# Performance work log

Measured on AMD Instinct MI355X. Metric: run time of the kernel, lower is better.

## Reference

```python
import jax, jax.numpy as jnp
import numpy as np

B, S, W = 32, 256, 32
T = 16               # topics per doc, each spanning L = S//T sentences
VOCAB, E, H, D = 400001, 300, 128, 128


def _gru_scan(x, Wih, Whh, bih, bhh, reverse=False):
    """x: [B,S,E] -> (outputs [B,S,H], final hidden [B,H]). Torch GRU cell math."""
    h0 = jnp.zeros((x.shape[0], Whh.shape[1]), x.dtype)
    gi_all = jnp.einsum('bse,ge->bsg', x, Wih) + bih  # precompute input gates [B,S,3H]

    def step(h, gi):
        gh = h @ Whh.T + bhh
        ir, iz, inn = jnp.split(gi, 3, axis=-1)
        hr, hz, hn = jnp.split(gh, 3, axis=-1)
        r = jax.nn.sigmoid(ir + hr)
        z = jax.nn.sigmoid(iz + hz)
        n = jnp.tanh(inn + r * hn)
        h_new = (1.0 - z) * n + z * h
        return h_new, h_new

    hT, hs = jax.lax.scan(step, h0, jnp.swapaxes(gi_all, 0, 1), reverse=reverse)
    return jnp.swapaxes(hs, 0, 1), hT


def setup_inputs() -> dict:
    key = jax.random.key(0)
    ks = jax.random.split(key, 16)
    sc_i = 1.0 / np.sqrt(H)
    L = S // T
    starts = (jnp.arange(T, dtype=jnp.int32) * L + 1)          # 1-based inclusive
    ends = (jnp.arange(T, dtype=jnp.int32) + 1) * L
    tse = jnp.broadcast_to(jnp.stack([starts, ends], axis=-1)[None], (B, T, 2)).astype(jnp.int32)
    return {
        'word_ids': jax.random.randint(ks[0], (B, S, W), 0, VOCAB, dtype=jnp.int32),
        'topic_start_ends': tse,
        'embed_table': jax.random.normal(ks[1], (VOCAB, E), jnp.float32) * 0.6,
        'Wih_f': jax.random.normal(ks[2], (3 * H, E), jnp.float32) * sc_i,
        'Whh_f': jax.random.normal(ks[3], (3 * H, H), jnp.float32) * sc_i,
        'bih_f': jax.random.normal(ks[4], (3 * H,), jnp.float32) * sc_i,
        'bhh_f': jax.random.normal(ks[5], (3 * H,), jnp.float32) * sc_i,
        'Wih_b': jax.random.normal(ks[6], (3 * H, E), jnp.float32) * sc_i,
        'Whh_b': jax.random.normal(ks[7], (3 * H, H), jnp.float32) * sc_i,
        'bih_b': jax.random.normal(ks[8], (3 * H,), jnp.float32) * sc_i,
        'bhh_b': jax.random.normal(ks[9], (3 * H,), jnp.float32) * sc_i,
        'v_attention': jax.random.normal(ks[10], (4 * H, 1), jnp.float32),
        'W_attention': jax.random.normal(ks[11], (4 * H, 4 * H), jnp.float32) * (1.0 / np.sqrt(4 * H)),
        'W1': jax.random.normal(ks[12], (D, 4 * H), jnp.float32) * (1.0 / np.sqrt(4 * H)),
        'b1': jax.random.normal(ks[13], (D,), jnp.float32) * 0.01,
        'W2': jax.random.normal(ks[14], (1, D), jnp.float32) * (1.0 / np.sqrt(D)),
        'b2': jax.random.normal(ks[15], (1,), jnp.float32) * 0.01,
    }


def reference(word_ids, topic_start_ends, embed_table,
              Wih_f, Whh_f, bih_f, bhh_f, Wih_b, Whh_b, bih_b, bhh_b,
              v_attention, W_attention, W1, b1, W2, b2):
    b, s, _ = word_ids.shape
    h = Whh_f.shape[1]
    # --- sent_encoder: gather word embeddings, mean-pool per sentence ---
    sent_emb = jnp.mean(embed_table[word_ids], axis=2)          # [B,S,E]
    # --- doc_encoder: bi-GRU ---
    out_f, hT_f = _gru_scan(sent_emb, Wih_f, Whh_f, bih_f, bhh_f, reverse=False)
    out_b, hT_b = _gru_scan(sent_emb, Wih_b, Whh_b, bih_b, bhh_b, reverse=True)
    sent_rep = jnp.concatenate([out_f, out_b], axis=-1)         # [B,S,2H]
    # faithful to hidden.view(batch_size, 2H) on hidden of shape [2,B,H]
    doc_vec = jnp.stack([hT_f, hT_b], axis=0).reshape(b, 2 * h)
    doc_rep = jnp.broadcast_to(doc_vec[:, None, :], (b, s, 2 * h))
    # topic reps via segment difference of cumulative GRU states (pad trick)
    pad = jnp.pad(sent_rep, ((0, 0), (1, 1), (0, 0)))           # [B,S+2,2H]
    starts = topic_start_ends[:, :, 0]                          # [B,T], 1-based
    ends = topic_start_ends[:, :, 1]

    def gat(idx, lo, hi):
        return jnp.take_along_axis(pad[..., lo:hi], idx[:, :, None], axis=1)
    fwd_part = gat(ends, 0, h) - gat(starts - 1, 0, h)
    bwd_part = gat(starts, h, 2 * h) - gat(ends + 1, h, 2 * h)
    topic_mat = jnp.concatenate([fwd_part, bwd_part], axis=-1)  # [B,T,2H]
    # scatter topic vectors to sentences: topic id = #starts at or before sentence
    sidx = jnp.arange(s, dtype=starts.dtype)
    topic_id = jnp.sum(sidx[None, :, None] >= (starts - 1)[:, None, :], axis=-1) - 1  # [B,S]
    topic_rep = jnp.take_along_axis(topic_mat, topic_id[:, :, None], axis=1)          # [B,S,2H]
    # --- decoder ---
    cat_ds = jnp.concatenate([doc_rep, sent_rep], axis=-1)      # [B,S,4H]
    cat_ts = jnp.concatenate([topic_rep, sent_rep], axis=-1)
    doc_scores = jnp.tanh(cat_ds @ W_attention) @ v_attention   # [B,S,1]
    topic_scores = jnp.tanh(cat_ts @ W_attention) @ v_attention
    doc_w = jax.nn.softmax(doc_scores, axis=1)
    topic_w = jax.nn.softmax(topic_scores, axis=1)
    context = doc_w * doc_rep + topic_w * topic_rep             # [B,S,2H]
    inp = jnp.concatenate([sent_rep, context], axis=-1)         # [B,S,4H]
    hdd = jax.nn.relu(inp @ W1.T + b1)                          # dropout = identity (eval)
    logits = (hdd @ W2.T + b2).squeeze(-1)                      # [B,S]
    return logits
```

## Files before the change

kernel.cpp:

```cpp
#include <hip/hip_runtime.h>
#include <hip/hip_bf16.h>
#include <cstdint>

#define Bk 32
#define Sk 256
#define Wk 32
#define Tk 16
#define Ek 300
#define Hk 128
#define Dk 128
#define NROWS (Bk*Sk)
#define GI_N  (3*Hk*2)
#define KPAD  320

typedef __attribute__((ext_vector_type(8))) short short8v;
typedef __attribute__((ext_vector_type(4))) float f32x4;

__device__ __forceinline__ float fast_sigmoid(float x) {
    return 1.f / (1.f + __expf(-x));
}
__device__ __forceinline__ float fast_tanh(float x) {
    float ax = fabsf(x);
    float e = __expf(2.f * ax);
    float t = 1.f - 2.f / (1.f + e);
    return copysignf(t, x);
}
__device__ __forceinline__ void barrier_lgkm() {
    asm volatile("s_waitcnt lgkmcnt(0)" ::: "memory");
    __builtin_amdgcn_s_barrier();
}
__device__ __forceinline__ void fma44(const float4& a, const float4& b, float (&c)[4][4]) {
    c[0][0]=fmaf(a.x,b.x,c[0][0]); c[0][1]=fmaf(a.x,b.y,c[0][1]); c[0][2]=fmaf(a.x,b.z,c[0][2]); c[0][3]=fmaf(a.x,b.w,c[0][3]);
    c[1][0]=fmaf(a.y,b.x,c[1][0]); c[1][1]=fmaf(a.y,b.y,c[1][1]); c[1][2]=fmaf(a.y,b.z,c[1][2]); c[1][3]=fmaf(a.y,b.w,c[1][3]);
    c[2][0]=fmaf(a.z,b.x,c[2][0]); c[2][1]=fmaf(a.z,b.y,c[2][1]); c[2][2]=fmaf(a.z,b.z,c[2][2]); c[2][3]=fmaf(a.z,b.w,c[2][3]);
    c[3][0]=fmaf(a.w,b.x,c[3][0]); c[3][1]=fmaf(a.w,b.y,c[3][1]); c[3][2]=fmaf(a.w,b.z,c[3][2]); c[3][3]=fmaf(a.w,b.w,c[3][3]);
}
__device__ __forceinline__ unsigned short f2bf(float f) {
    uint32_t u = __float_as_uint(f);
    uint32_t r = (u + 0x7FFFu + ((u >> 16) & 1u)) >> 16;
    return (unsigned short)r;
}
__device__ __forceinline__ float bf2f(unsigned short h) {
    return __uint_as_float(((uint32_t)h) << 16);
}

__global__ __launch_bounds__(256) void pack_kernel(
    const float* __restrict__ Wf, const float* __restrict__ Wb,
    const float* __restrict__ bf, const float* __restrict__ bb,
    const float* __restrict__ Watt, const float* __restrict__ W1,
    unsigned short* __restrict__ Bgt_hi, unsigned short* __restrict__ Bgt_lo,
    float* __restrict__ bias_gi, unsigned short* __restrict__ Wswt,
    float* __restrict__ BW1)
{
    int idx = blockIdx.x * 256 + threadIdx.x;
    if (idx < 768 * KPAD) {
        int n = idx / KPAD, k = idx % KPAD;
        float v = 0.f;
        if (k < 300) v = (n < 384) ? Wf[n * 300 + k] : Wb[(n - 384) * 300 + k];
        unsigned short h = f2bf(v);
        Bgt_hi[idx] = h;
        Bgt_lo[idx] = f2bf(v - bf2f(h));
    }
    if (idx < 768) bias_gi[idx] = (idx < 384) ? bf[idx] : bb[idx - 384];
    if (idx < 512 * 256) {
        int n = idx >> 8, k = idx & 255;
        Wswt[idx] = f2bf(Watt[(size_t)(256 + k) * 512 + n]);
    }
    if (idx < 512 * 128) {
        int k = idx >> 7, n = idx & 127;
        BW1[idx] = W1[n * 512 + k];
    }
}

__global__ __launch_bounds__(256) void embed_mean_kernel(
    const int* __restrict__ wids, const float* __restrict__ table,
    unsigned short* __restrict__ Ahi, unsigned short* __restrict__ Alo)
{
    int wv = (blockIdx.x << 2) + (threadIdx.x >> 6);
    int lane = threadIdx.x & 63;
    if (wv >= NROWS) return;
    const int* idp = wids + (size_t)wv * Wk;
    float4 a0 = {0,0,0,0}, a1 = {0,0,0,0};
    #pragma unroll 4
    for (int w = 0; w < Wk; ++w) {
        int id = idp[w];
        const float4* r4 = reinterpret_cast<const float4*>(table + (size_t)id * Ek);
        float4 v0 = r4[lane];
        a0.x += v0.x; a0.y += v0.y; a0.z += v0.z; a0.w += v0.w;
        if (lane < 11) {
            float4 v1 = r4[64 + lane];
            a1.x += v1.x; a1.y += v1.y; a1.z += v1.z; a1.w += v1.w;
        }
    }
    const float sc = 1.f / 32.f;
    unsigned short* hp = Ahi + (size_t)wv * KPAD;
    unsigned short* lp = Alo + (size_t)wv * KPAD;
    {
        float v[4] = {a0.x*sc, a0.y*sc, a0.z*sc, a0.w*sc};
        ushort4 h, l;
        h.x=f2bf(v[0]); h.y=f2bf(v[1]); h.z=f2bf(v[2]); h.w=f2bf(v[3]);
        l.x=f2bf(v[0]-bf2f(h.x)); l.y=f2bf(v[1]-bf2f(h.y));
        l.z=f2bf(v[2]-bf2f(h.z)); l.w=f2bf(v[3]-bf2f(h.w));
        *reinterpret_cast<ushort4*>(hp + lane*4) = h;
        *reinterpret_cast<ushort4*>(lp + lane*4) = l;
    }
    if (lane < 11) {
        float v[4] = {a1.x*sc, a1.y*sc, a1.z*sc, a1.w*sc};
        ushort4 h, l;
        h.x=f2bf(v[0]); h.y=f2bf(v[1]); h.z=f2bf(v[2]); h.w=f2bf(v[3]);
        l.x=f2bf(v[0]-bf2f(h.x)); l.y=f2bf(v[1]-bf2f(h.y));
        l.z=f2bf(v[2]-bf2f(h.z)); l.w=f2bf(v[3]-bf2f(h.w));
        *reinterpret_cast<ushort4*>(hp + 256 + lane*4) = h;
        *reinterpret_cast<ushort4*>(lp + 256 + lane*4) = l;
    } else if (lane < 16) {
        ushort4 z = {0,0,0,0};
        *reinterpret_cast<ushort4*>(hp + 256 + lane*4) = z;
        *reinterpret_cast<ushort4*>(lp + 256 + lane*4) = z;
    }
}

__global__ __launch_bounds__(256) void cvt_bf16_kernel(
    const float* __restrict__ src, unsigned short* __restrict__ dst, int n8)
{
    int i = blockIdx.x * 256 + threadIdx.x;
    if (i >= n8) return;
    const float4* s = reinterpret_cast<const float4*>(src) + (size_t)i * 2;
    float4 v0 = s[0], v1 = s[1];
    unsigned short r[8];
    r[0]=f2bf(v0.x); r[1]=f2bf(v0.y); r[2]=f2bf(v0.z); r[3]=f2bf(v0.w);
    r[4]=f2bf(v1.x); r[5]=f2bf(v1.y); r[6]=f2bf(v1.z); r[7]=f2bf(v1.w);
    *reinterpret_cast<short8v*>(dst + (size_t)i * 8) = *reinterpret_cast<short8v*>(r);
}

template<int PASSES, bool BIAS>
__global__ __launch_bounds__(256) void mfma_gemm_kernel(
    const unsigned short* __restrict__ Ahi, const unsigned short* __restrict__ Alo,
    const unsigned short* __restrict__ Bthi, const unsigned short* __restrict__ Btlo,
    const float* __restrict__ bias, float* __restrict__ C,
    int M, int N, int Kp)
{
    __shared__ unsigned short At_h[128][40];
    __shared__ unsigned short Bt_h[128][40];
    __shared__ unsigned short At_l[128][40];
    __shared__ unsigned short Bt_l[128][40];
    const int tid = threadIdx.x;
    const int m0 = blockIdx.x * 128, n0 = blockIdx.y * 128;
    const int lane = tid & 63;
    const int wave = tid >> 6;
    const int wr = (wave >> 1) * 64, wc = (wave & 1) * 64;
    const int l15 = lane & 15, l4 = lane >> 4;
    f32x4 acc[4][4] = {};

    const int srow = tid >> 1;
    const int scol = (tid & 1) * 16;

    for (int k0 = 0; k0 < Kp; k0 += 32) {
        {
            const unsigned short* ag = Ahi + (size_t)(m0 + srow) * Kp + k0 + scol;
            *reinterpret_cast<short8v*>(&At_h[srow][scol])     = *reinterpret_cast<const short8v*>(ag);
            *reinterpret_cast<short8v*>(&At_h[srow][scol + 8]) = *reinterpret_cast<const short8v*>(ag + 8);
            const unsigned short* bg = Bthi + (size_t)(n0 + srow) * Kp + k0 + scol;
            *reinterpret_cast<short8v*>(&Bt_h[srow][scol])     = *reinterpret_cast<const short8v*>(bg);
            *reinterpret_cast<short8v*>(&Bt_h[srow][scol + 8]) = *reinterpret_cast<const short8v*>(bg + 8);
            if (PASSES > 1) {
                const unsigned short* ag2 = Alo + (size_t)(m0 + srow) * Kp + k0 + scol;
                *reinterpret_cast<short8v*>(&At_l[srow][scol])     = *reinterpret_cast<const short8v*>(ag2);
                *reinterpret_cast<short8v*>(&At_l[srow][scol + 8]) = *reinterpret_cast<const short8v*>(ag2 + 8);
                const unsigned short* bg2 = Btlo + (size_t)(n0 + srow) * Kp + k0 + scol;
                *reinterpret_cast<short8v*>(&Bt_l[srow][scol])     = *reinterpret_cast<const short8v*>(bg2);
                *reinterpret_cast<short8v*>(&Bt_l[srow][scol + 8]) = *reinterpret_cast<const short8v*>(bg2 + 8);
            }
        }
        __syncthreads();
        short8v a_h[4], b_h[4], a_l[4], b_l[4];
        #pragma unroll
        for (int f = 0; f < 4; ++f) {
            a_h[f] = *reinterpret_cast<const short8v*>(&At_h[wr + f*16 + l15][l4*8]);
            b_h[f] = *reinterpret_cast<const short8v*>(&Bt_h[wc + f*16 + l15][l4*8]);
            if (PASSES > 1) {
                a_l[f] = *reinterpret_cast<const short8v*>(&At_l[wr + f*16 + l15][l4*8]);
                b_l[f] = *reinterpret_cast<const short8v*>(&Bt_l[wc + f*16 + l15][l4*8]);
            }
        }
        #pragma unroll
        for (int i = 0; i < 4; ++i) {
            #pragma unroll
            for (int j = 0; j < 4; ++j) {
                acc[i][j] = __builtin_amdgcn_mfma_f32_16x16x32_bf16(a_h[i], b_h[j], acc[i][j], 0, 0, 0);
                if (PASSES > 1) {
                    acc[i][j] = __builtin_amdgcn_mfma_f32_16x16x32_bf16(a_l[i], b_h[j], acc[i][j], 0, 0, 0);
                    acc[i][j] = __builtin_amdgcn_mfma_f32_16x16x32_bf16(a_h[i], b_l[j], acc[i][j], 0, 0, 0);
                }
            }
        }
        __syncthreads();
    }
    #pragma unroll
    for (int i = 0; i < 4; ++i) {
        #pragma unroll
        for (int j = 0; j < 4; ++j) {
            int col = n0 + wc + j * 16 + l15;
            float badd = BIAS ? bias[col] : 0.f;
            #pragma unroll
            for (int r = 0; r < 4; ++r) {
                int row = m0 + wr + i * 16 + l4 * 4 + r;
                C[(size_t)row * N + col] = acc[i][j][r] + badd;
            }
        }
    }
}

template<bool BIAS, bool RELU>
__global__ __launch_bounds__(256) void gemm_kernel(
    const float* __restrict__ A, const float* __restrict__ B,
    const float* __restrict__ bias, float* __restrict__ C,
    int M, int N, int K)
{
    __shared__ float As[64][68];
    __shared__ float Bs[64][68];
    const int tid = threadIdx.x;
    const int m0 = blockIdx.x * 64;
    const int n0 = blockIdx.y * 64;
    const int tx = tid & 15, ty = tid >> 4;
    const int lr = tid >> 2;
    const int lc = tid & 3;
    float acc[4][4] = {};

    for (int k0 = 0; k0 < K; k0 += 64) {
        #pragma unroll
        for (int i = 0; i < 4; ++i) {
            int kk = lc * 4 + i * 16;
            int gm = m0 + lr;
            int gk = k0 + kk;
            float4 v = {0,0,0,0};
            if (gm < M && gk < K)
                v = *reinterpret_cast<const float4*>(A + (size_t)gm * K + gk);
            As[kk+0][lr] = v.x; As[kk+1][lr] = v.y; As[kk+2][lr] = v.z; As[kk+3][lr] = v.w;
        }
        #pragma unroll
        for (int i = 0; i < 4; ++i) {
            int nn = lc * 4 + i * 16;
            int gk = k0 + lr;
            float4 v = {0,0,0,0};
            if (gk < K)
                v = *reinterpret_cast<const float4*>(B + (size_t)gk * N + n0 + nn);
            *reinterpret_cast<float4*>(&Bs[lr][nn]) = v;
        }
        __syncthreads();
        #pragma unroll 8
        for (int k = 0; k < 64; ++k) {
            float4 av = *reinterpret_cast<const float4*>(&As[k][ty*4]);
            float4 bv = *reinterpret_cast<const float4*>(&Bs[k][tx*4]);
            fma44(av, bv, acc);
        }
        __syncthreads();
    }
    #pragma unroll
    for (int r = 0; r < 4; ++r) {
        int row = m0 + ty * 4 + r;
        if (row < M) {
            float4 v = {acc[r][0], acc[r][1], acc[r][2], acc[r][3]};
            if (BIAS) {
                const float* bp = bias + n0 + tx * 4;
                v.x += bp[0]; v.y += bp[1]; v.z += bp[2]; v.w += bp[3];
            }
            if (RELU) {
                v.x = fmaxf(v.x, 0.f); v.y = fmaxf(v.y, 0.f);
                v.z = fmaxf(v.z, 0.f); v.w = fmaxf(v.w, 0.f);
            }
            *reinterpret_cast<float4*>(C + (size_t)row * N + n0 + tx * 4) = v;
        }
    }
}

__global__ __launch_bounds__(512, 1) void gru_scan_kernel(
    const float* __restrict__ gi,
    const float* __restrict__ Whh_f, const float* __restrict__ Whh_b,
    const float* __restrict__ bhh_f, const float* __restrict__ bhh_b,
    float* __restrict__ sent_rep,
    float* __restrict__ hT)
{
    const int blk = blockIdx.x;
    const int dir = blk >> 5;
    const int b   = blk & 31;
    const int t = threadIdx.x;
    const int lane = t & 63;
    const int w_id = t >> 6;
    const int q = lane >> 4;
    const int m = lane & 15;
    const int j = w_id * 16 + m;
    const float* Whh = dir ? Whh_b : Whh_f;
    const float* bhh = dir ? bhh_b : bhh_f;
    __shared__ float hbufA[144];
    __shared__ float hbufB[144];

    const float* wr0 = Whh + (size_t)j * 128 + 32 * q;
    const float* wr1 = wr0 + 128 * 128;
    const float* wr2 = wr0 + 256 * 128;
    float4 wA0 = *reinterpret_cast<const float4*>(wr0 +  0);
    float4 wA1 = *reinterpret_cast<const float4*>(wr0 +  4);
    float4 wA2 = *reinterpret_cast<const float4*>(wr0 +  8);
    float4 wA3 = *reinterpret_cast<const float4*>(wr0 + 12);
    float4 wA4 = *reinterpret_cast<const float4*>(wr0 + 16);
    float4 wA5 = *reinterpret_cast<const float4*>(wr0 + 20);
    float4 wA6 = *reinterpret_cast<const float4*>(wr0 + 24);
    float4 wA7 = *reinterpret_cast<const float4*>(wr0 + 28);
    float4 wB0 = *reinterpret_cast<const float4*>(wr1 +  0);
    float4 wB1 = *reinterpret_cast<const float4*>(wr1 +  4);
    float4 wB2 = *reinterpret_cast<const float4*>(wr1 +  8);
    float4 wB3 = *reinterpret_cast<const float4*>(wr1 + 12);
    float4 wB4 = *reinterpret_cast<const float4*>(wr1 + 16);
    float4 wB5 = *reinterpret_cast<const float4*>(wr1 + 20);
    float4 wB6 = *reinterpret_cast<const float4*>(wr1 + 24);
    float4 wB7 = *reinterpret_cast<const float4*>(wr1 + 28);
    float4 wC0 = *reinterpret_cast<const float4*>(wr2 +  0);
    float4 wC1 = *reinterpret_cast<const float4*>(wr2 +  4);
    float4 wC2 = *reinterpret_cast<const float4*>(wr2 +  8);
    float4 wC3 = *reinterpret_cast<const float4*>(wr2 + 12);
    float4 wC4 = *reinterpret_cast<const float4*>(wr2 + 16);
    float4 wC5 = *reinterpret_cast<const float4*>(wr2 + 20);
    float4 wC6 = *reinterpret_cast<const float4*>(wr2 + 24);
    float4 wC7 = *reinterpret_cast<const float4*>(wr2 + 28);
    const float br = bhh[j];
    const float bz = bhh[128 + j];
    const float bn = bhh[256 + j];

    if (t < 144) { hbufA[t] = 0.f; hbufB[t] = 0.f; }

    const int ji = 36 * (j >> 5) + (j & 31);
    const float* gbase = gi + (size_t)(b * Sk) * GI_N + dir * 384 + j;
    float hold = 0.f;
    float gir = 0.f, giz = 0.f, gin_ = 0.f;
    {
        const int s0 = dir ? (Sk - 1) : 0;
        const float* gp = gbase + (size_t)s0 * GI_N;
        gir = gp[0]; giz = gp[128]; gin_ = gp[256];
    }
    __syncthreads();

    #define STEP(RD, WR, SEXPR) { \
        const int s = (SEXPR); \
        const float4* hseg = reinterpret_cast<const float4*>(RD) + 9 * q; \
        float pA = 0.f, pB = 0.f, pC = 0.f; \
        { float4 h4; \
          h4 = hseg[0]; \
          pA=fmaf(wA0.x,h4.x,pA); pA=fmaf(wA0.y,h4.y,pA); pA=fmaf(wA0.z,h4.z,pA); pA=fmaf(wA0.w,h4.w,pA); \
          pB=fmaf(wB0.x,h4.x,pB); pB=fmaf(wB0.y,h4.y,pB); pB=fmaf(wB0.z,h4.z,pB); pB=fmaf(wB0.w,h4.w,pB); \
          pC=fmaf(wC0.x,h4.x,pC); pC=fmaf(wC0.y,h4.y,pC); pC=fmaf(wC0.z,h4.z,pC); pC=fmaf(wC0.w,h4.w,pC); \
          h4 = hseg[1]; \
          pA=fmaf(wA1.x,h4.x,pA); pA=fmaf(wA1.y,h4.y,pA); pA=fmaf(wA1.z,h4.z,pA); pA=fmaf(wA1.w,h4.w,pA); \
          pB=fmaf(wB1.x,h4.x,pB); pB=fmaf(wB1.y,h4.y,pB); pB=fmaf(wB1.z,h4.z,pB); pB=fmaf(wB1.w,h4.w,pB); \
          pC=fmaf(wC1.x,h4.x,pC); pC=fmaf(wC1.y,h4.y,pC); pC=fmaf(wC1.z,h4.z,pC); pC=fmaf(wC1.w,h4.w,pC); \
          h4 = hseg[2]; \
          pA=fmaf(wA2.x,h4.x,pA); pA=fmaf(wA2.y,h4.y,pA); pA=fmaf(wA2.z,h4.z,pA); pA=fmaf(wA2.w,h4.w,pA); \
          pB=fmaf(wB2.x,h4.x,pB); pB=fmaf(wB2.y,h4.y,pB); pB=fmaf(wB2.z,h4.z,pB); pB=fmaf(wB2.w,h4.w,pB); \
          pC=fmaf(wC2.x,h4.x,pC); pC=fmaf(wC2.y,h4.y,pC); pC=fmaf(wC2.z,h4.z,pC); pC=fmaf(wC2.w,h4.w,pC); \
          h4 = hseg[3]; \
          pA=fmaf(wA3.x,h4.x,pA); pA=fmaf(wA3.y,h4.y,pA); pA=fmaf(wA3.z,h4.z,pA); pA=fmaf(wA3.w,h4.w,pA); \
          pB=fmaf(wB3.x,h4.x,pB); pB=fmaf(wB3.y,h4.y,pB); pB=fmaf(wB3.z,h4.z,pB); pB=fmaf(wB3.w,h4.w,pB); \
          pC=fmaf(wC3.x,h4.x,pC); pC=fmaf(wC3.y,h4.y,pC); pC=fmaf(wC3.z,h4.z,pC); pC=fmaf(wC3.w,h4.w,pC); \
          h4 = hseg[4]; \
          pA=fmaf(wA4.x,h4.x,pA); pA=fmaf(wA4.y,h4.y,pA); pA=fmaf(wA4.z,h4.z,pA); pA=fmaf(wA4.w,h4.w,pA); \
          pB=fmaf(wB4.x,h4.x,pB); pB=fmaf(wB4.y,h4.y,pB); pB=fmaf(wB4.z,h4.z,pB); pB=fmaf(wB4.w,h4.w,pB); \
          pC=fmaf(wC4.x,h4.x,pC); pC=fmaf(wC4.y,h4.y,pC); pC=fmaf(wC4.z,h4.z,pC); pC=fmaf(wC4.w,h4.w,pC); \
          h4 = hseg[5]; \
          pA=fmaf(wA5.x,h4.x,pA); pA=fmaf(wA5.y,h4.y,pA); pA=fmaf(wA5.z,h4.z,pA); pA=fmaf(wA5.w,h4.w,pA); \
          pB=fmaf(wB5.x,h4.x,pB); pB=fmaf(wB5.y,h4.y,pB); pB=fmaf(wB5.z,h4.z,pB); pB=fmaf(wB5.w,h4.w,pB); \
          pC=fmaf(wC5.x,h4.x,pC); pC=fmaf(wC5.y,h4.y,pC); pC=fmaf(wC5.z,h4.z,pC); pC=fmaf(wC5.w,h4.w,pC); \
          h4 = hseg[6]; \
          pA=fmaf(wA6.x,h4.x,pA); pA=fmaf(wA6.y,h4.y,pA); pA=fmaf(wA6.z,h4.z,pA); pA=fmaf(wA6.w,h4.w,pA); \
          pB=fmaf(wB6.x,h4.x,pB); pB=fmaf(wB6.y,h4.y,pB); pB=fmaf(wB6.z,h4.z,pB); pB=fmaf(wB6.w,h4.w,pB); \
          pC=fmaf(wC6.x,h4.x,pC); pC=fmaf(wC6.y,h4.y,pC); pC=fmaf(wC6.z,h4.z,pC); pC=fmaf(wC6.w,h4.w,pC); \
          h4 = hseg[7]; \
          pA=fmaf(wA7.x,h4.x,pA); pA=fmaf(wA7.y,h4.y,pA); pA=fmaf(wA7.z,h4.z,pA); pA=fmaf(wA7.w,h4.w,pA); \
          pB=fmaf(wB7.x,h4.x,pB); pB=fmaf(wB7.y,h4.y,pB); pB=fmaf(wB7.z,h4.z,pB); pB=fmaf(wB7.w,h4.w,pB); \
          pC=fmaf(wC7.x,h4.x,pC); pC=fmaf(wC7.y,h4.y,pC); pC=fmaf(wC7.z,h4.z,pC); pC=fmaf(wC7.w,h4.w,pC); } \
        pA += __shfl_xor(pA, 16); pA += __shfl_xor(pA, 32); \
        pB += __shfl_xor(pB, 16); pB += __shfl_xor(pB, 32); \
        pC += __shfl_xor(pC, 16); pC += __shfl_xor(pC, 32); \
        if (q == 0) { \
            float r = fast_sigmoid(gir + pA + br); \
            float z = fast_sigmoid(giz + pB + bz); \
            float n = fast_tanh(gin_ + r * (pC + bn)); \
            hold = (1.f - z) * n + z * hold; \
            (WR)[ji] = hold; \
            sent_rep[(size_t)(b * Sk + s) * 256 + dir * 128 + j] = hold; \
            const int sn = dir ? (s > 0 ? s - 1 : 0) : (s + 1 < Sk ? s + 1 : Sk - 1); \
            const float* gp = gbase + (size_t)sn * GI_N; \
            gir = gp[0]; giz = gp[128]; gin_ = gp[256]; \
        } \
        barrier_lgkm(); \
    }

    for (int step = 0; step < Sk; step += 2) {
        STEP(hbufA, hbufB, dir ? (Sk - 1 - step) : step);
        STEP(hbufB, hbufA, dir ? (Sk - 2 - step) : (step + 1));
    }
    #undef STEP

    if (q == 0) hT[dir * 4096 + b * 128 + j] = hold;
}

__device__ __forceinline__ float4 sr_load_guard(const float* sr, int b, int sidx, int j4) {
    if (sidx < 0 || sidx >= Sk) { float4 z = {0,0,0,0}; return z; }
    return reinterpret_cast<const float4*>(sr)[(size_t)(b * Sk + sidx) * 64 + j4];
}
__global__ __launch_bounds__(64) void prep_kernel(
    const int* __restrict__ tse, const float* __restrict__ sent_rep,
    const float* __restrict__ hT, float* __restrict__ dvtm)
{
    const int b = blockIdx.x;
    const int t = blockIdx.y;
    const int j4 = threadIdx.x;
    if (t == 16) {
        int dir = b >> 4;
        int bb = 2 * (b & 15) + (j4 >> 5);
        int jj4 = j4 & 31;
        float4 v = reinterpret_cast<const float4*>(hT)[dir * 1024 + bb * 32 + jj4];
        reinterpret_cast<float4*>(dvtm)[b * 64 + j4] = v;
    } else {
        int st = tse[b * 32 + t * 2];
        int en = tse[b * 32 + t * 2 + 1];
        float4 va, vb;
        if (j4 < 32) {
            va = sr_load_guard(sent_rep, b, en - 1, j4);
            vb = sr_load_guard(sent_rep, b, st - 2, j4);
        } else {
            va = sr_load_guard(sent_rep, b, st - 1, j4);
            vb = sr_load_guard(sent_rep, b, en, j4);
        }
        float4 v = {va.x - vb.x, va.y - vb.y, va.z - vb.z, va.w - vb.w};
        reinterpret_cast<float4*>(dvtm)[(32 + b * 16 + t) * 64 + j4] = v;
    }
}

__global__ __launch_bounds__(256) void scores_kernel(
    const float* __restrict__ SW,
    const float* __restrict__ dptp,
    const float* __restrict__ vatt,
    const int* __restrict__ tse,
    float* __restrict__ dsc, float* __restrict__ tsc)
{
    int row = (blockIdx.x << 2) + (threadIdx.x >> 6);
    int lane = threadIdx.x & 63;
    if (row >= NROWS) return;
    int b = row >> 8, s = row & 255;
    int ti = 0;
    #pragma unroll
    for (int t = 1; t < 16; ++t) ti += (s >= tse[b * 32 + t * 2] - 1) ? 1 : 0;
    const float4* swr = reinterpret_cast<const float4*>(SW + (size_t)row * 512);
    const float4* dpr = reinterpret_cast<const float4*>(dptp + (size_t)b * 512);
    const float4* tpr = reinterpret_cast<const float4*>(dptp + (size_t)(32 + b * 16 + ti) * 512);
    const float4* vv  = reinterpret_cast<const float4*>(vatt);
    float sd = 0.f, st = 0.f;
    #pragma unroll
    for (int q = 0; q < 2; ++q) {
        int i = lane * 2 + q;
        float4 sw = swr[i], dp = dpr[i], tp = tpr[i], v = vv[i];
        sd += fast_tanh(sw.x + dp.x) * v.x + fast_tanh(sw.y + dp.y) * v.y
            + fast_tanh(sw.z + dp.z) * v.z + fast_tanh(sw.w + dp.w) * v.w;
        st += fast_tanh(sw.x + tp.x) * v.x + fast_tanh(sw.y + tp.y) * v.y
            + fast_tanh(sw.z + tp.z) * v.z + fast_tanh(sw.w + tp.w) * v.w;
    }
    #pragma unroll
    for (int off = 32; off; off >>= 1) {
        sd += __shfl_xor(sd, off);
        st += __shfl_xor(st, off);
    }
    if (lane == 0) { dsc[row] = sd; tsc[row] = st; }
}

__global__ __launch_bounds__(256) void softmax_kernel(float* __restrict__ dsc, float* __restrict__ tsc)
{
    const int b = blockIdx.x, sidx = threadIdx.x;
    const int lane = sidx & 63, wid = sidx >> 6;
    __shared__ float rd[4], rt[4];
    float d = dsc[b * Sk + sidx];
    float t = tsc[b * Sk + sidx];
    float md = d, mt = t;
    #pragma unroll
    for (int off = 32; off; off >>= 1) {
        md = fmaxf(md, __shfl_xor(md, off));
        mt = fmaxf(mt, __shfl_xor(mt, off));
    }
    if (lane == 0) { rd[wid] = md; rt[wid] = mt; }
    __syncthreads();
    md = fmaxf(fmaxf(rd[0], rd[1]), fmaxf(rd[2], rd[3]));
    mt = fmaxf(fmaxf(rt[0], rt[1]), fmaxf(rt[2], rt[3]));
    float ed = __expf(d - md), et = __expf(t - mt);
    float sd = ed, stt = et;
    #pragma unroll
    for (int off = 32; off; off >>= 1) {
        sd += __shfl_xor(sd, off);
        stt += __shfl_xor(stt, off);
    }
    __syncthreads();
    if (lane == 0) { rd[wid] = sd; rt[wid] = stt; }
    __syncthreads();
    sd = rd[0] + rd[1] + rd[2] + rd[3];
    stt = rt[0] + rt[1] + rt[2] + rt[3];
    dsc[b * Sk + sidx] = ed / sd;
    tsc[b * Sk + sidx] = et / stt;
}

__global__ __launch_bounds__(128) void build_inp_kernel(
    const float* __restrict__ sent_rep, const float* __restrict__ dvtm,
    const float* __restrict__ dw, const float* __restrict__ tw,
    const int* __restrict__ tse, float* __restrict__ inp)
{
    int row = blockIdx.x;
    int b = row >> 8, s = row & 255;
    int f4c = threadIdx.x;
    float4 v;
    if (f4c < 64) {
        v = reinterpret_cast<const float4*>(sent_rep)[(size_t)row * 64 + f4c];
    } else {
        int ti = 0;
        #pragma unroll
        for (int t = 1; t < 16; ++t) ti += (s >= tse[b * 32 + t * 2] - 1) ? 1 : 0;
        float dwv = dw[row], twv = tw[row];
        int j4 = f4c - 64;
        float4 dv = reinterpret_cast<const float4*>(dvtm)[b * 64 + j4];
        float4 tm = reinterpret_cast<const float4*>(dvtm)[(32 + b * 16 + ti) * 64 + j4];
        v.x = dwv * dv.x + twv * tm.x;
        v.y = dwv * dv.y + twv * tm.y;
        v.z = dwv * dv.z + twv * tm.z;
        v.w = dwv * dv.w + twv * tm.w;
    }
    reinterpret_cast<float4*>(inp)[(size_t)row * 128 + f4c] = v;
}

__global__ __launch_bounds__(256) void logits_kernel(
    const float* __restrict__ hdd, const float* __restrict__ W2,
    const float* __restrict__ b2, float* __restrict__ out)
{
    int row = (blockIdx.x << 2) + (threadIdx.x >> 6);
    int lane = threadIdx.x & 63;
    if (row >= NROWS) return;
    float acc = hdd[(size_t)row * 128 + lane] * W2[lane]
              + hdd[(size_t)row * 128 + 64 + lane] * W2[64 + lane];
    #pragma unroll
    for (int off = 32; off; off >>= 1) acc += __shfl_xor(acc, off);
    if (lane == 0) out[row] = acc + b2[0];
}

extern "C" void kernel_launch(void* const* d_in, const int* in_sizes, int n_in,
                              void* d_out, int out_size, void* d_ws, size_t ws_size,
                              hipStream_t stream)
{
    const int*   wids  = (const int*)d_in[0];
    const int*   tse   = (const int*)d_in[1];
    const float* table = (const float*)d_in[2];
    const float* Wihf  = (const float*)d_in[3];
    const float* Whhf  = (const float*)d_in[4];
    const float* bihf  = (const float*)d_in[5];
    const float* bhhf  = (const float*)d_in[6];
    const float* Wihb  = (const float*)d_in[7];
    const float* Whhb  = (const float*)d_in[8];
    const float* bihb  = (const float*)d_in[9];
    const float* bhhb  = (const float*)d_in[10];
    const float* vatt  = (const float*)d_in[11];
    const float* Watt  = (const float*)d_in[12];
    const float* W1    = (const float*)d_in[13];
    const float* b1    = (const float*)d_in[14];
    const float* W2    = (const float*)d_in[15];
    const float* b2    = (const float*)d_in[16];
    float* ws = (float*)d_ws;
    float* out = (float*)d_out;

    unsigned short* Ahi   = (unsigned short*)(ws + 0);
    unsigned short* Alo   = (unsigned short*)(ws + 1310720);
    float* gi             = ws + 2621440;
    float* sent_rep       = ws + 8912896;
    unsigned short* SRhi  = (unsigned short*)(ws + 11010048);
    float* hT             = ws + 12058624;
    float* dvtm           = ws + 12066816;
    float* dptp           = ws + 12206080;
    float* dsc            = ws + 12484608;
    float* tsc            = ws + 12492800;
    unsigned short* BgtH  = (unsigned short*)(ws + 12500992);
    unsigned short* BgtL  = (unsigned short*)(ws + 12623872);
    float* bias_gi        = ws + 12746752;
    unsigned short* Wswt  = (unsigned short*)(ws + 12747520);
    float* BW1            = ws + 12813056;
    float* SW             = ws + 12878592;
    float* inp            = ws + 0;
    float* hdd            = ws + 4194304;

    if (ws_size < (size_t)17072896 * sizeof(float)) return;

    pack_kernel<<<960, 256, 0, stream>>>(Wihf, Wihb, bihf, bihb, Watt, W1,
                                         BgtH, BgtL, bias_gi, Wswt, BW1);
    embed_mean_kernel<<<2048, 256, 0, stream>>>(wids, table, Ahi, Alo);
    mfma_gemm_kernel<3, true><<<dim3(64, 6), 256, 0, stream>>>(
        Ahi, Alo, BgtH, BgtL, bias_gi, gi, NROWS, 768, KPAD);
    gru_scan_kernel<<<64, 512, 0, stream>>>(gi, Whhf, Whhb, bhhf, bhhb, sent_rep, hT);
    cvt_bf16_kernel<<<1024, 256, 0, stream>>>(sent_rep, SRhi, NROWS * 256 / 8);
    prep_kernel<<<dim3(32, 17), 64, 0, stream>>>(tse, sent_rep, hT, dvtm);
    mfma_gemm_kernel<1, false><<<dim3(64, 4), 256, 0, stream>>>(
        SRhi, nullptr, Wswt, nullptr, nullptr, SW, NROWS, 512, 256);
    gemm_kernel<false,false><<<dim3(9, 8), 256, 0, stream>>>(dvtm, Watt, nullptr, dptp, 544, 512, 256);
    scores_kernel<<<2048, 256, 0, stream>>>(SW, dptp, vatt, tse, dsc, tsc);
    softmax_kernel<<<32, 256, 0, stream>>>(dsc, tsc);
    build_inp_kernel<<<NROWS, 128, 0, stream>>>(sent_rep, dvtm, dsc, tsc, tse, inp);
    gemm_kernel<true,true><<<dim3(128, 2), 256, 0, stream>>>(inp, BW1, b1, hdd, NROWS, 128, 512);
    logits_kernel<<<2048, 256, 0, stream>>>(hdd, W2, b2, out);
}
```

Before: 345.6 us.

## Fuse attention score epilogue into MFMA GEMM and move W1 GEMM to split-bf16 MFMA

The SW=sent_rep·W_att GEMM now computes tanh-and-dot with v_attention directly in its epilogue. It writes per-slot partial doc and topic scores, so the 8192x512 fp32 SW matrix is never written and read back. The softmax sums the 8 partials. The final W1 layer switches from the fp32 SIMT GEMM to a 3-pass hi/lo bf16 MFMA GEMM with fused bias and ReLU, and build_inp emits split bf16 inputs. A small kernel precomputes the topic-id map once instead of recomputing it in several kernels. The W1 GEMM launches only 64 blocks, which may underfill the GPU.

```diff
diff --git a/kernel.cpp b/kernel.cpp
--- a/kernel.cpp
+++ b/kernel.cpp
@@ -50,7 +50,7 @@
     const float* __restrict__ Watt, const float* __restrict__ W1,
     unsigned short* __restrict__ Bgt_hi, unsigned short* __restrict__ Bgt_lo,
     float* __restrict__ bias_gi, unsigned short* __restrict__ Wswt,
-    float* __restrict__ BW1)
+    unsigned short* __restrict__ W1H, unsigned short* __restrict__ W1L)
 {
     int idx = blockIdx.x * 256 + threadIdx.x;
     if (idx < 768 * KPAD) {
@@ -66,9 +66,11 @@
         int n = idx >> 8, k = idx & 255;
         Wswt[idx] = f2bf(Watt[(size_t)(256 + k) * 512 + n]);
     }
-    if (idx < 512 * 128) {
-        int k = idx >> 7, n = idx & 127;
-        BW1[idx] = W1[n * 512 + k];
+    if (idx < 128 * 512) {
+        float v = W1[idx];
+        unsigned short h = f2bf(v);
+        W1H[idx] = h;
+        W1L[idx] = f2bf(v - bf2f(h));
     }
 }
 
@@ -132,7 +134,7 @@
     *reinterpret_cast<short8v*>(dst + (size_t)i * 8) = *reinterpret_cast<short8v*>(r);
 }
 
-template<int PASSES, bool BIAS>
+template<int PASSES, bool BIAS, bool RELU>
 __global__ __launch_bounds__(256) void mfma_gemm_kernel(
     const unsigned short* __restrict__ Ahi, const unsigned short* __restrict__ Alo,
     const unsigned short* __restrict__ Bthi, const unsigned short* __restrict__ Btlo,
@@ -204,7 +206,90 @@
             #pragma unroll
             for (int r = 0; r < 4; ++r) {
                 int row = m0 + wr + i * 16 + l4 * 4 + r;
-                C[(size_t)row * N + col] = acc[i][j][r] + badd;
+                float v = acc[i][j][r] + badd;
+                if (RELU) v = fmaxf(v, 0.f);
+                C[(size_t)row * N + col] = v;
+            }
+        }
+    }
+}
+
+__global__ __launch_bounds__(256) void mfma_swscore_kernel(
+    const unsigned short* __restrict__ Ahi, const unsigned short* __restrict__ Bthi,
+    const float* __restrict__ dptp, const float* __restrict__ vatt,
+    const int* __restrict__ tidmap,
+    float* __restrict__ dscp, float* __restrict__ tscp)
+{
+    __shared__ unsigned short At_h[128][40];
+    __shared__ unsigned short Bt_h[128][40];
+    const int tid = threadIdx.x;
+    const int m0 = blockIdx.x * 128, n0 = blockIdx.y * 128;
+    const int Kp = 256, N = 512;
+    (void)N;
+    const int lane = tid & 63;
+    const int wave = tid >> 6;
+    const int wr = (wave >> 1) * 64, wc = (wave & 1) * 64;
+    const int l15 = lane & 15, l4 = lane >> 4;
+    f32x4 acc[4][4] = {};
+
+    const int srow = tid >> 1;
+    const int scol = (tid & 1) * 16;
+
+    for (int k0 = 0; k0 < Kp; k0 += 32) {
+        {
+            const unsigned short* ag = Ahi + (size_t)(m0 + srow) * Kp + k0 + scol;
+            *reinterpret_cast<short8v*>(&At_h[srow][scol])     = *reinterpret_cast<const short8v*>(ag);
+            *reinterpret_cast<short8v*>(&At_h[srow][scol + 8]) = *reinterpret_cast<const short8v*>(ag + 8);
+            const unsigned short* bg = Bthi + (size_t)(n0 + srow) * Kp + k0 + scol;
+            *reinterpret_cast<short8v*>(&Bt_h[srow][scol])     = *reinterpret_cast<const short8v*>(bg);
+            *reinterpret_cast<short8v*>(&Bt_h[srow][scol + 8]) = *reinterpret_cast<const short8v*>(bg + 8);
+        }
+        __syncthreads();
+        short8v a_h[4], b_h[4];
+        #pragma unroll
+        for (int f = 0; f < 4; ++f) {
+            a_h[f] = *reinterpret_cast<const short8v*>(&At_h[wr + f*16 + l15][l4*8]);
+            b_h[f] = *reinterpret_cast<const short8v*>(&Bt_h[wc + f*16 + l15][l4*8]);
+        }
+        #pragma unroll
+        for (int i = 0; i < 4; ++i)
+            #pragma unroll
+            for (int j = 0; j < 4; ++j)
+                acc[i][j] = __builtin_amdgcn_mfma_f32_16x16x32_bf16(a_h[i], b_h[j], acc[i][j], 0, 0, 0);
+        __syncthreads();
+    }
+    const int bb = m0 >> 8;
+    const float* dpr = dptp + (size_t)bb * 512;
+    float vv[4], dpv[4];
+    #pragma unroll
+    for (int j = 0; j < 4; ++j) {
+        int col = n0 + wc + j * 16 + l15;
+        vv[j] = vatt[col];
+        dpv[j] = dpr[col];
+    }
+    const int slot = blockIdx.y * 2 + (wc >> 6);
+    #pragma unroll
+    for (int i = 0; i < 4; ++i) {
+        #pragma unroll
+        for (int r = 0; r < 4; ++r) {
+            int row = m0 + wr + i * 16 + l4 * 4 + r;
+            int ti = tidmap[row];
+            const float* tpr = dptp + (size_t)(32 + bb * 16 + ti) * 512;
+            float sd = 0.f, st = 0.f;
+            #pragma unroll
+            for (int j = 0; j < 4; ++j) {
+                int col = n0 + wc + j * 16 + l15;
+                float c = acc[i][j][r];
+                sd += fast_tanh(c + dpv[j]) * vv[j];
+                st += fast_tanh(c + tpr[col]) * vv[j];
+            }
+            sd += __shfl_xor(sd, 1); sd += __shfl_xor(sd, 2);
+            sd += __shfl_xor(sd, 4); sd += __shfl_xor(sd, 8);
+            st += __shfl_xor(st, 1); st += __shfl_xor(st, 2);
+            st += __shfl_xor(st, 4); st += __shfl_xor(st, 8);
+            if (l15 == 0) {
+                dscp[(size_t)row * 8 + slot] = sd;
+                tscp[(size_t)row * 8 + slot] = st;
             }
         }
     }
@@ -277,8 +362,7 @@
     const float* __restrict__ gi,
     const float* __restrict__ Whh_f, const float* __restrict__ Whh_b,
     const float* __restrict__ bhh_f, const float* __restrict__ bhh_b,
-    float* __restrict__ sent_rep,
-    float* __restrict__ hT)
+    float* __restrict__ sent_rep, float* __restrict__ hT)
 {
     const int blk = blockIdx.x;
     const int dir = blk >> 5;
@@ -434,49 +518,28 @@
     }
 }
 
-__global__ __launch_bounds__(256) void scores_kernel(
-    const float* __restrict__ SW,
-    const float* __restrict__ dptp,
-    const float* __restrict__ vatt,
-    const int* __restrict__ tse,
+__global__ __launch_bounds__(256) void topic_map_kernel(
+    const int* __restrict__ tse, int* __restrict__ tidmap)
+{
+    const int b = blockIdx.x, s = threadIdx.x;
+    int ti = 0;
+    #pragma unroll
+    for (int t = 1; t < 16; ++t) ti += (s >= tse[b * 32 + t * 2] - 1) ? 1 : 0;
+    tidmap[b * 256 + s] = ti;
+}
+
+__global__ __launch_bounds__(256) void softmax_kernel(
+    const float* __restrict__ dscp, const float* __restrict__ tscp,
     float* __restrict__ dsc, float* __restrict__ tsc)
-{
-    int row = (blockIdx.x << 2) + (threadIdx.x >> 6);
-    int lane = threadIdx.x & 63;
-    if (row >= NROWS) return;
-    int b = row >> 8, s = row & 255;
-    int ti = 0;
-    #pragma unroll
-    for (int t = 1; t < 16; ++t) ti += (s >= tse[b * 32 + t * 2] - 1) ? 1 : 0;
-    const float4* swr = reinterpret_cast<const float4*>(SW + (size_t)row * 512);
-    const float4* dpr = reinterpret_cast<const float4*>(dptp + (size_t)b * 512);
-    const float4* tpr = reinterpret_cast<const float4*>(dptp + (size_t)(32 + b * 16 + ti) * 512);
-    const float4* vv  = reinterpret_cast<const float4*>(vatt);
-    float sd = 0.f, st = 0.f;
-    #pragma unroll
-    for (int q = 0; q < 2; ++q) {
-        int i = lane * 2 + q;
-        float4 sw = swr[i], dp = dpr[i], tp = tpr[i], v = vv[i];
-        sd += fast_tanh(sw.x + dp.x) * v.x + fast_tanh(sw.y + dp.y) * v.y
-            + fast_tanh(sw.z + dp.z) * v.z + fast_tanh(sw.w + dp.w) * v.w;
-        st += fast_tanh(sw.x + tp.x) * v.x + fast_tanh(sw.y + tp.y) * v.y
-            + fast_tanh(sw.z + tp.z) * v.z + fast_tanh(sw.w + tp.w) * v.w;
-    }
-    #pragma unroll
-    for (int off = 32; off; off >>= 1) {
-        sd += __shfl_xor(sd, off);
-        st += __shfl_xor(st, off);
-    }
-    if (lane == 0) { dsc[row] = sd; tsc[row] = st; }
-}
-
-__global__ __launch_bounds__(256) void softmax_kernel(float* __restrict__ dsc, float* __restrict__ tsc)
 {
     const int b = blockIdx.x, sidx = threadIdx.x;
     const int lane = sidx & 63, wid = sidx >> 6;
     __shared__ float rd[4], rt[4];
-    float d = dsc[b * Sk + sidx];
-    float t = tsc[b * Sk + sidx];
+    const float4* dp8 = reinterpret_cast<const float4*>(dscp + (size_t)(b * Sk + sidx) * 8);
+    const float4* tp8 = reinterpret_cast<const float4*>(tscp + (size_t)(b * Sk + sidx) * 8);
+    float4 d0 = dp8[0], d1 = dp8[1], t0 = tp8[0], t1 = tp8[1];
+    float d = ((d0.x + d0.y) + (d0.z + d0.w)) + ((d1.x + d1.y) + (d1.z + d1.w));
+    float t = ((t0.x + t0.y) + (t0.z + t0.w)) + ((t1.x + t1.y) + (t1.z + t1.w));
     float md = d, mt = t;
     #pragma unroll
     for (int off = 32; off; off >>= 1) {
@@ -506,18 +569,17 @@
 __global__ __launch_bounds__(128) void build_inp_kernel(
     const float* __restrict__ sent_rep, const float* __restrict__ dvtm,
     const float* __restrict__ dw, const float* __restrict__ tw,
-    const int* __restrict__ tse, float* __restrict__ inp)
+    const int* __restrict__ tidmap,
+    unsigned short* __restrict__ inpH, unsigned short* __restrict__ inpL)
 {
     int row = blockIdx.x;
-    int b = row >> 8, s = row & 255;
+    int b = row >> 8;
     int f4c = threadIdx.x;
     float4 v;
     if (f4c < 64) {
         v = reinterpret_cast<const float4*>(sent_rep)[(size_t)row * 64 + f4c];
     } else {
-        int ti = 0;
-        #pragma unroll
-        for (int t = 1; t < 16; ++t) ti += (s >= tse[b * 32 + t * 2] - 1) ? 1 : 0;
+        int ti = tidmap[row];
         float dwv = dw[row], twv = tw[row];
         int j4 = f4c - 64;
         float4 dv = reinterpret_cast<const float4*>(dvtm)[b * 64 + j4];
@@ -527,7 +589,12 @@
         v.z = dwv * dv.z + twv * tm.z;
         v.w = dwv * dv.w + twv * tm.w;
     }
-    reinterpret_cast<float4*>(inp)[(size_t)row * 128 + f4c] = v;
+    ushort4 h, l;
+    h.x = f2bf(v.x); h.y = f2bf(v.y); h.z = f2bf(v.z); h.w = f2bf(v.w);
+    l.x = f2bf(v.x - bf2f(h.x)); l.y = f2bf(v.y - bf2f(h.y));
+    l.z = f2bf(v.z - bf2f(h.z)); l.w = f2bf(v.w - bf2f(h.w));
+    *reinterpret_cast<ushort4*>(inpH + (size_t)row * 512 + f4c * 4) = h;
+    *reinterpret_cast<ushort4*>(inpL + (size_t)row * 512 + f4c * 4) = l;
 }
 
 __global__ __launch_bounds__(256) void logits_kernel(
@@ -582,27 +649,32 @@
     unsigned short* BgtL  = (unsigned short*)(ws + 12623872);
     float* bias_gi        = ws + 12746752;
     unsigned short* Wswt  = (unsigned short*)(ws + 12747520);
-    float* BW1            = ws + 12813056;
-    float* SW             = ws + 12878592;
-    float* inp            = ws + 0;
+    unsigned short* W1H   = (unsigned short*)(ws + 12813056);
+    unsigned short* W1L   = (unsigned short*)(ws + 12845824);
+    float* dscp           = ws + 12878592;
+    float* tscp           = ws + 12944128;
+    int*   tidmap         = (int*)(ws + 13009664);
+    unsigned short* inpH  = (unsigned short*)(ws + 0);
+    unsigned short* inpL  = (unsigned short*)(ws + 2097152);
     float* hdd            = ws + 4194304;
 
-    if (ws_size < (size_t)17072896 * sizeof(float)) return;
+    if (ws_size < (size_t)13017856 * sizeof(float)) return;
 
     pack_kernel<<<960, 256, 0, stream>>>(Wihf, Wihb, bihf, bihb, Watt, W1,
-                                         BgtH, BgtL, bias_gi, Wswt, BW1);
+                                         BgtH, BgtL, bias_gi, Wswt, W1H, W1L);
     embed_mean_kernel<<<2048, 256, 0, stream>>>(wids, table, Ahi, Alo);
-    mfma_gemm_kernel<3, true><<<dim3(64, 6), 256, 0, stream>>>(
+    mfma_gemm_kernel<3, true, false><<<dim3(64, 6), 256, 0, stream>>>(
         Ahi, Alo, BgtH, BgtL, bias_gi, gi, NROWS, 768, KPAD);
     gru_scan_kernel<<<64, 512, 0, stream>>>(gi, Whhf, Whhb, bhhf, bhhb, sent_rep, hT);
     cvt_bf16_kernel<<<1024, 256, 0, stream>>>(sent_rep, SRhi, NROWS * 256 / 8);
     prep_kernel<<<dim3(32, 17), 64, 0, stream>>>(tse, sent_rep, hT, dvtm);
-    mfma_gemm_kernel<1, false><<<dim3(64, 4), 256, 0, stream>>>(
-        SRhi, nullptr, Wswt, nullptr, nullptr, SW, NROWS, 512, 256);
+    topic_map_kernel<<<32, 256, 0, stream>>>(tse, tidmap);
     gemm_kernel<false,false><<<dim3(9, 8), 256, 0, stream>>>(dvtm, Watt, nullptr, dptp, 544, 512, 256);
-    scores_kernel<<<2048, 256, 0, stream>>>(SW, dptp, vatt, tse, dsc, tsc);
-    softmax_kernel<<<32, 256, 0, stream>>>(dsc, tsc);
-    build_inp_kernel<<<NROWS, 128, 0, stream>>>(sent_rep, dvtm, dsc, tsc, tse, inp);
-    gemm_kernel<true,true><<<dim3(128, 2), 256, 0, stream>>>(inp, BW1, b1, hdd, NROWS, 128, 512);
+    mfma_swscore_kernel<<<dim3(64, 4), 256, 0, stream>>>(
+        SRhi, Wswt, dptp, vatt, tidmap, dscp, tscp);
+    softmax_kernel<<<32, 256, 0, stream>>>(dscp, tscp, dsc, tsc);
+    build_inp_kernel<<<NROWS, 128, 0, stream>>>(sent_rep, dvtm, dsc, tsc, tidmap, inpH, inpL);
+    mfma_gemm_kernel<3, true, true><<<dim3(64, 1), 256, 0, stream>>>(
+        inpH, inpL, W1H, W1L, b1, hdd, NROWS, 128, 512);
     logits_kernel<<<2048, 256, 0, stream>>>(hdd, W2, b2, out);
 }
```

Result: no change. 339.0 us (-1.9%).
